# Optimization experiments

Hardware: AMD Instinct MI355X
Metric: run time of the kernel (lower is better)

## Reference

```python
import jax, jax.numpy as jnp
import numpy as np

N = 100_000      # nodes
D = 64           # in_dim
E = 1_600_000    # edges (avg degree 16)
P_L = 0.5        # leaky slope for low-pass gate
P_H = 0.5        # leaky slope for high-pass gate


def setup_inputs() -> dict:
    key = jax.random.key(0)
    ks = jax.random.split(key, 10)
    h = jax.random.normal(ks[0], (N, D), jnp.float32)
    d = jax.random.uniform(ks[1], (N,), jnp.float32)  # degree norms 1/sqrt(deg)
    src = jax.random.randint(ks[2], (E,), 0, N)
    dst = jax.random.randint(ks[3], (E,), 0, N)
    # xavier_normal(gain=1.414) scale ~ gain*sqrt(2/(fan_in+fan_out))
    sg = 1.414 * np.sqrt(2.0 / (2 * D + 1))
    sr = 1.414 * np.sqrt(2.0 / (2 * D + D))
    Wl = jax.random.normal(ks[4], (1, 2 * D), jnp.float32) * sg
    bl = jnp.zeros((1,), jnp.float32)
    Wh = jax.random.normal(ks[5], (1, 2 * D), jnp.float32) * sg
    bh = jnp.zeros((1,), jnp.float32)
    Wr = jax.random.normal(ks[6], (D, 2 * D), jnp.float32) * sr
    br = jnp.zeros((D,), jnp.float32)
    return {"h": h, "d": d, "src": src, "dst": dst,
            "Wl": Wl, "bl": bl, "Wh": Wh, "bh": bh, "Wr": Wr, "br": br}


def reference(h, d, src, dst, Wl, bl, Wh, bh, Wr, br):
    # gate_x(cat([h_dst, h_src])) == h_dst @ W[:, :D] + h_src @ W[:, D:] + b
    # -> project once per node [N], gather per edge [E] (avoids [E,2D] concat)
    low_dst = h @ Wl[0, :D]
    low_src = h @ Wl[0, D:]
    _low = low_dst[dst] + low_src[src] + bl[0]                     # [E]
    g_low = jnp.tanh(jax.nn.relu(jnp.where(_low > 0, _low, -P_L * _low)))

    high_dst = h @ Wh[0, :D]
    high_src = h @ Wh[0, D:]
    _high = high_dst[dst] + high_src[src] + bh[0]                  # [E]
    g_high = jnp.tanh(-jax.nn.relu(jnp.where(_high > 0, _high, -P_H * _high)))

    dd = d[dst] * d[src]                                           # [E]
    e_low = g_low * dd
    e_high = g_high * dd

    h_src = h[src]                                                 # [E, D]
    z_low = jax.ops.segment_sum(h_src * e_low[:, None], dst, num_segments=N)
    z_high = jax.ops.segment_sum(h_src * e_high[:, None], dst, num_segments=N)

    z = jnp.concatenate([z_low, z_high], axis=1)                   # [N, 2D]
    return z @ Wr.T + br                                           # [N, D]
```

## Files before the change

### kernel.cpp

```cpp
#include <hip/hip_runtime.h>
#include <hip/hip_fp16.h>
#include <math.h>

#define N_NODES 100000
#define D_DIM   64
#define N_EDGES 1600000
#define P_L 0.5f
#define P_H 0.5f

#define NPB   32
#define NB    3125
#define TILE  2048
#define NT    784
#define GRP   28
#define GT    28
#define CAPB  768
#define CAPH  512
#define ZS    132


typedef unsigned int uint;
typedef unsigned short ushort_t;
typedef float f2 __attribute__((ext_vector_type(2)));

__device__ inline ushort_t f2bf(float f) {
    uint u = __float_as_uint(f);
    uint r = (u + 0x7fffu + ((u >> 16) & 1u)) >> 16;
    return (ushort_t)r;
}

__device__ inline float tanh_pos(float x) {
    return 1.f - 2.f / (__expf(2.f * x) + 1.f);
}

__device__ inline void fma16(uint gy, uint4 hv, f2* acc) {
    float el = __half2float(__ushort_as_half((unsigned short)(gy & 0xffffu)));
    float eh = __half2float(__ushort_as_half((unsigned short)(gy >> 16)));
    f2 f01 = {__uint_as_float(hv.x << 16), __uint_as_float(hv.x & 0xffff0000u)};
    f2 f23 = {__uint_as_float(hv.y << 16), __uint_as_float(hv.y & 0xffff0000u)};
    f2 f45 = {__uint_as_float(hv.z << 16), __uint_as_float(hv.z & 0xffff0000u)};
    f2 f67 = {__uint_as_float(hv.w << 16), __uint_as_float(hv.w & 0xffff0000u)};
    acc[0] += f01 * el; acc[1] += f23 * el; acc[2] += f45 * el; acc[3] += f67 * el;
    acc[4] += f01 * eh; acc[5] += f23 * eh; acc[6] += f45 * eh; acc[7] += f67 * eh;
}

__device__ inline unsigned long long match4(int dl, bool active) {
    unsigned long long m = __ballot(active);
    #pragma unroll
    for (int b = 0; b < 4; ++b) {
        unsigned long long bal = __ballot(active && ((dl >> b) & 1));
        m &= ((dl >> b) & 1) ? bal : ~bal;
    }
    return m;
}

__global__ __launch_bounds__(256) void node_gates_kernel(
    const float* __restrict__ h, const float* __restrict__ dvec,
    const float* __restrict__ Wl, const float* __restrict__ Wh,
    ushort_t* __restrict__ hbf,
    float4* __restrict__ gdst4, float4* __restrict__ gsrc4)
{
    int tid = threadIdx.x;
    int lane = tid & 63;
    int half = lane >> 5;
    int l32 = lane & 31;
    int node = blockIdx.x * 8 + (tid >> 6) * 2 + half;

    float2 hv2 = *(const float2*)(h + (size_t)node * 64 + l32 * 2);
    uint pk = (uint)f2bf(hv2.x) | ((uint)f2bf(hv2.y) << 16);
    ((uint*)hbf)[(size_t)node * 32 + l32] = pk;

    float pld = hv2.x * Wl[2 * l32]      + hv2.y * Wl[2 * l32 + 1];
    float pls = hv2.x * Wl[64 + 2 * l32] + hv2.y * Wl[64 + 2 * l32 + 1];
    float phd = hv2.x * Wh[2 * l32]      + hv2.y * Wh[2 * l32 + 1];
    float phs = hv2.x * Wh[64 + 2 * l32] + hv2.y * Wh[64 + 2 * l32 + 1];
    #pragma unroll
    for (int m = 16; m >= 1; m >>= 1) {
        pld += __shfl_xor(pld, m);
        pls += __shfl_xor(pls, m);
        phd += __shfl_xor(phd, m);
        phs += __shfl_xor(phs, m);
    }
    if (l32 == 0) {
        float d = dvec[node];
        gdst4[node] = make_float4(pld, phd, d, 0.f);
        gsrc4[node] = make_float4(pls, phs, d, 0.f);
    }
}

__global__ __launch_bounds__(512) void bucket_hist_kernel(const int* __restrict__ dst,
                                                          int* __restrict__ T) {
    __shared__ int hist[NB];
    int tid = threadIdx.x;
    for (int i = tid; i < NB; i += 512) hist[i] = 0;
    __syncthreads();
    int base = blockIdx.x * TILE;
    #pragma unroll
    for (int j = 0; j < TILE / 512; ++j) {
        int e = base + j * 512 + tid;
        if (e < N_EDGES) atomicAdd(&hist[dst[e] >> 5], 1);
    }
    __syncthreads();
    int* row = T + (size_t)blockIdx.x * NB;
    for (int i = tid; i < NB; i += 512) row[i] = hist[i];
}

__global__ __launch_bounds__(1024) void scanA1_kernel(int* __restrict__ T,
                                                      int* __restrict__ S) {
    int b = blockIdx.x * 1024 + threadIdx.x;
    if (b >= NB) return;
    int g = blockIdx.y;
    int run = 0;
    #pragma unroll
    for (int w = g * GT; w < g * GT + GT; ++w) {
        int idx = w * NB + b;
        int v = T[idx];
        T[idx] = run;
        run += v;
    }
    S[(size_t)g * NB + b] = run;
}

__global__ __launch_bounds__(1024) void scanA2_kernel(int* __restrict__ S,
                                                      int* __restrict__ totG) {
    int b = blockIdx.x * 1024 + threadIdx.x;
    if (b >= NB) return;
    int run = 0;
    #pragma unroll
    for (int g = 0; g < GRP; ++g) {
        int idx = g * NB + b;
        int v = S[idx];
        S[idx] = run;
        run += v;
    }
    totG[b] = run;
}

__global__ __launch_bounds__(1024) void scanB_kernel(const int* __restrict__ totG,
                                                     int* __restrict__ baseG,
                                                     int* __restrict__ bucketoffs,
                                                     const float* __restrict__ Wr,
                                                     float* __restrict__ wrt) {
    int tid = threadIdx.x;
    for (int idx = tid; idx < 64 * 128; idx += 1024) {
        int c = idx >> 7;
        int k = idx & 127;
        wrt[k * 64 + c] = Wr[idx];
    }

    __shared__ int scan_lds[1024];
    int a[4];
    int s = 0;
    #pragma unroll
    for (int i = 0; i < 4; ++i) {
        int b = tid * 4 + i;
        a[i] = (b < NB) ? totG[b] : 0;
        s += a[i];
    }
    scan_lds[tid] = s;
    __syncthreads();
    for (int d = 1; d < 1024; d <<= 1) {
        int v = (tid >= d) ? scan_lds[tid - d] : 0;
        __syncthreads();
        scan_lds[tid] += v;
        __syncthreads();
    }
    int excl = scan_lds[tid] - s;
    int total = scan_lds[1023];
    #pragma unroll
    for (int i = 0; i < 4; ++i) {
        int b = tid * 4 + i;
        if (b < NB) { baseG[b] = excl; bucketoffs[b] = excl; }
        excl += a[i];
    }
    if (tid == 0) bucketoffs[NB] = total;
}

__global__ __launch_bounds__(512) void place_kernel(
    const int* __restrict__ src, const int* __restrict__ dst,
    const int* __restrict__ T, const int* __restrict__ S,
    const int* __restrict__ baseG,
    const float4* __restrict__ gdst4, const float4* __restrict__ gsrc4,
    const float* __restrict__ bl, const float* __restrict__ bh,
    uint2* __restrict__ ebuf)
{
    __shared__ int cur[NB];
    int tid = threadIdx.x;
    const int* row  = T + (size_t)blockIdx.x * NB;
    const int* Srow = S + (size_t)(blockIdx.x / GT) * NB;
    for (int i = tid; i < NB; i += 512) cur[i] = row[i] + Srow[i] + baseG[i];
    __syncthreads();

    float bl0 = bl[0], bh0 = bh[0];
    int base = blockIdx.x * TILE;
    #pragma unroll
    for (int j = 0; j < TILE / 512; ++j) {
        int e = base + j * 512 + tid;
        if (e >= N_EDGES) continue;
        int t = dst[e];
        int s = src[e];
        float4 gt = gdst4[t];
        float4 gs = gsrc4[s];
        float xl = gt.x + gs.x + bl0;
        float xh = gt.y + gs.y + bh0;
        float ll = xl > 0.f ? xl : -P_L * xl;
        float hh = xh > 0.f ? xh : -P_H * xh;
        float dd = gt.z * gs.z;
        float el =  tanh_pos(ll) * dd;
        float eh = -tanh_pos(hh) * dd;
        uint ge = (uint)__half_as_ushort(__float2half_rn(el))
                | ((uint)__half_as_ushort(__float2half_rn(eh)) << 16);
        int b  = t >> 5;
        uint dl = (uint)(t & 31);
        int pos = atomicAdd(&cur[b], 1);
        ebuf[pos] = make_uint2((uint)s | (dl << 17), ge);
    }
}

__global__ __launch_bounds__(256) void accum_final_kernel(
    const int* __restrict__ bucketoffs, const uint2* __restrict__ ebuf,
    const ushort_t* __restrict__ hbf, const float* __restrict__ wrt,
    const float* __restrict__ br, float* __restrict__ out)
{
    __shared__ float z[16 * ZS];
    __shared__ uint2 srec[CAPH];
    __shared__ int ncount[16];
    __shared__ int nbase[16];
    __shared__ int ncur[16];

    int tid = threadIdx.x;
    int lane = tid & 63;
    int bk = blockIdx.x >> 1;
    int hf = blockIdx.x & 1;
    int beg = bucketoffs[bk];
    int end = bucketoffs[bk + 1];
    int cnt = end - beg;
    if (cnt > CAPB) cnt = CAPB;

    if (tid < 16) ncount[tid] = 0;

    bool hA = tid < cnt;
    bool hB = tid + 256 < cnt;
    bool hC = tid + 512 < cnt;
    uint2 rA = hA ? ebuf[beg + tid]       : make_uint2(0, 0);
    uint2 rB = hB ? ebuf[beg + tid + 256] : make_uint2(0, 0);
    uint2 rC = hC ? ebuf[beg + tid + 512] : make_uint2(0, 0);
    __syncthreads();

    int dA5 = (int)((rA.x >> 17) & 31u);
    int dB5 = (int)((rB.x >> 17) & 31u);
    int dC5 = (int)((rC.x >> 17) & 31u);
    bool oA = hA && ((dA5 >> 4) == hf);
    bool oB = hB && ((dB5 >> 4) == hf);
    bool oC = hC && ((dC5 >> 4) == hf);
    int dlA = dA5 & 15, dlB = dB5 & 15, dlC = dC5 & 15;

    unsigned long long mA = match4(dlA, oA);
    if (oA && lane == (int)__builtin_ctzll(mA))
        atomicAdd(&ncount[dlA], (int)__popcll(mA));
    unsigned long long mB = match4(dlB, oB);
    if (oB && lane == (int)__builtin_ctzll(mB))
        atomicAdd(&ncount[dlB], (int)__popcll(mB));
    unsigned long long mC = match4(dlC, oC);
    if (oC && lane == (int)__builtin_ctzll(mC))
        atomicAdd(&ncount[dlC], (int)__popcll(mC));
    __syncthreads();

    if (tid < 16) {
        int v = ncount[tid];
        int p = v;
        #pragma unroll
        for (int d = 1; d < 16; d <<= 1) {
            int x = __shfl_up(p, d);
            if (tid >= d) p += x;
        }
        nbase[tid] = p - v;
        ncur[tid]  = p - v;
    }
    __syncthreads();

    if (oA) {
        int ldr = (int)__builtin_ctzll(mA);
        int base = 0;
        if (lane == ldr) base = atomicAdd(&ncur[dlA], (int)__popcll(mA));
        base = __shfl(base, ldr);
        int pos = base + (int)__popcll(mA & ((1ull << lane) - 1ull));
        if (pos < CAPH) srec[pos] = rA;
    }
    if (oB) {
        int ldr = (int)__builtin_ctzll(mB);
        int base = 0;
        if (lane == ldr) base = atomicAdd(&ncur[dlB], (int)__popcll(mB));
        base = __shfl(base, ldr);
        int pos = base + (int)__popcll(mB & ((1ull << lane) - 1ull));
        if (pos < CAPH) srec[pos] = rB;
    }
    if (oC) {
        int ldr = (int)__builtin_ctzll(mC);
        int base = 0;
        if (lane == ldr) base = atomicAdd(&ncur[dlC], (int)__popcll(mC));
        base = __shfl(base, ldr);
        int pos = base + (int)__popcll(mC & ((1ull << lane) - 1ull));
        if (pos < CAPH) srec[pos] = rC;
    }
    __syncthreads();

    int sg = tid >> 3;
    int l8 = tid & 7;
    int node4 = sg >> 1;
    int par = sg & 1;
    int rbeg = nbase[node4];
    int rend = ncur[node4];
    if (rend > CAPH) rend = CAPH;

    f2 acc[8];
    #pragma unroll
    for (int j = 0; j < 8; ++j) acc[j] = (f2){0.f, 0.f};

    int k = rbeg + par;
    for (; k + 6 < rend; k += 8) {
        uint2 r0 = srec[k];
        uint2 r1 = srec[k + 2];
        uint2 r2 = srec[k + 4];
        uint2 r3 = srec[k + 6];
        uint4 h0 = *(const uint4*)(hbf + (size_t)(r0.x & 0x1FFFF) * 64 + l8 * 8);
        uint4 h1 = *(const uint4*)(hbf + (size_t)(r1.x & 0x1FFFF) * 64 + l8 * 8);
        uint4 h2 = *(const uint4*)(hbf + (size_t)(r2.x & 0x1FFFF) * 64 + l8 * 8);
        uint4 h3 = *(const uint4*)(hbf + (size_t)(r3.x & 0x1FFFF) * 64 + l8 * 8);
        fma16(r0.y, h0, acc);
        fma16(r1.y, h1, acc);
        fma16(r2.y, h2, acc);
        fma16(r3.y, h3, acc);
    }
    for (; k < rend; k += 2) {
        uint2 r0 = srec[k];
        uint4 hv = *(const uint4*)(hbf + (size_t)(r0.x & 0x1FFFF) * 64 + l8 * 8);
        fma16(r0.y, hv, acc);
    }

    float* zp = &z[node4 * ZS + l8 * 8];
    if (par == 0) {
        *(float4*)(zp + 0)  = make_float4(acc[0].x, acc[0].y, acc[1].x, acc[1].y);
        *(float4*)(zp + 4)  = make_float4(acc[2].x, acc[2].y, acc[3].x, acc[3].y);
        *(float4*)(zp + 64) = make_float4(acc[4].x, acc[4].y, acc[5].x, acc[5].y);
        *(float4*)(zp + 68) = make_float4(acc[6].x, acc[6].y, acc[7].x, acc[7].y);
    }
    __syncthreads();
    if (par == 1) {
        float4 z0 = *(float4*)(zp + 0);
        float4 z1 = *(float4*)(zp + 4);
        float4 z2 = *(float4*)(zp + 64);
        float4 z3 = *(float4*)(zp + 68);
        *(float4*)(zp + 0)  = make_float4(z0.x + acc[0].x, z0.y + acc[0].y, z0.z + acc[1].x, z0.w + acc[1].y);
        *(float4*)(zp + 4)  = make_float4(z1.x + acc[2].x, z1.y + acc[2].y, z1.z + acc[3].x, z1.w + acc[3].y);
        *(float4*)(zp + 64) = make_float4(z2.x + acc[4].x, z2.y + acc[4].y, z2.z + acc[5].x, z2.w + acc[5].y);
        *(float4*)(zp + 68) = make_float4(z3.x + acc[6].x, z3.y + acc[6].y, z3.z + acc[7].x, z3.w + acc[7].y);
    }
    __syncthreads();

    int node = tid >> 4;
    int g = tid & 15;
    f2 fa0 = {0.f, 0.f}, fa1 = {0.f, 0.f};
    const float* zrow = z + node * ZS;
    #pragma unroll 2
    for (int kk = 0; kk < 128; kk += 4) {
        float4 z4 = *(const float4*)(zrow + kk);
        const float* wp = wrt + kk * 64 + g * 4;
        float4 w0 = *(const float4*)(wp);
        float4 w1 = *(const float4*)(wp + 64);
        float4 w2 = *(const float4*)(wp + 128);
        float4 w3 = *(const float4*)(wp + 192);
        fa0 += (f2){w0.x, w0.y} * z4.x; fa1 += (f2){w0.z, w0.w} * z4.x;
        fa0 += (f2){w1.x, w1.y} * z4.y; fa1 += (f2){w1.z, w1.w} * z4.y;
        fa0 += (f2){w2.x, w2.y} * z4.z; fa1 += (f2){w2.z, w2.w} * z4.z;
        fa0 += (f2){w3.x, w3.y} * z4.w; fa1 += (f2){w3.z, w3.w} * z4.w;
    }
    int n = bk * NPB + hf * 16 + node;
    float* op = out + (size_t)n * 64 + g * 4;
    const float* bp = br + g * 4;
    *(float4*)(op) = make_float4(fa0.x + bp[0], fa0.y + bp[1], fa1.x + bp[2], fa1.y + bp[3]);
}

extern "C" void kernel_launch(void* const* d_in, const int* in_sizes, int n_in,
                              void* d_out, int out_size, void* d_ws, size_t ws_size,
                              hipStream_t stream) {
    const float* h    = (const float*)d_in[0];
    const float* dvec = (const float*)d_in[1];
    const int*   src  = (const int*)  d_in[2];
    const int*   dst  = (const int*)  d_in[3];
    const float* Wl   = (const float*)d_in[4];
    const float* bl   = (const float*)d_in[5];
    const float* Wh   = (const float*)d_in[6];
    const float* bh   = (const float*)d_in[7];
    const float* Wr   = (const float*)d_in[8];
    const float* br   = (const float*)d_in[9];
    float* out = (float*)d_out;

    char* ws = (char*)d_ws;
    size_t off = 0;
    auto alloc = [&](size_t bytes) { char* p = ws + off; off += (bytes + 255) & ~size_t(255); return p; };

    ushort_t* hbf       = (ushort_t*)alloc((size_t)N_NODES * 64 * 2);
    float4*   gdst4     = (float4*)  alloc((size_t)N_NODES * 16);
    float4*   gsrc4     = (float4*)  alloc((size_t)N_NODES * 16);
    float*    wrt       = (float*)   alloc(64 * 128 * 4);
    int*      T         = (int*)     alloc((size_t)NT * NB * 4);
    int*      S         = (int*)     alloc((size_t)GRP * NB * 4);
    int*      totG      = (int*)     alloc((size_t)NB * 4);
    int*      baseG     = (int*)     alloc((size_t)NB * 4);
    int*      bucketoffs= (int*)     alloc((size_t)(NB + 1) * 4);
    uint2*    ebuf      = (uint2*)   alloc((size_t)N_EDGES * 8);

    node_gates_kernel<<<N_NODES / 8, 256, 0, stream>>>(h, dvec, Wl, Wh, hbf, gdst4, gsrc4);
    bucket_hist_kernel<<<NT, 512, 0, stream>>>(dst, T);
    {
        dim3 g1((NB + 1023) / 1024, GRP);
        scanA1_kernel<<<g1, 1024, 0, stream>>>(T, S);
    }
    scanA2_kernel<<<(NB + 1023) / 1024, 1024, 0, stream>>>(S, totG);
    scanB_kernel<<<1, 1024, 0, stream>>>(totG, baseG, bucketoffs, Wr, wrt);
    place_kernel<<<NT, 512, 0, stream>>>(src, dst, T, S, baseG, gdst4, gsrc4, bl, bh, ebuf);
    accum_final_kernel<<<NB * 2, 256, 0, stream>>>(bucketoffs, ebuf, hbf, wrt, br, out);
}
```

Measured before the change: 285.4 us.

## Replace tiled histogram and multi-pass scan with padded global atomic counters

The per-tile shared-memory histogram plus the two-level column scan is replaced by one global atomic count per bucket, padded to separate cache lines, and the counters are zeroed inside the node gates kernel. The placement pass then uses global atomics on those counters instead of precomputed per-tile offsets, which removes two kernels and the large T/S workspace traffic. In exchange, every edge now issues global atomics twice, and edge order within a bucket becomes nondeterministic. The accumulation loop also gains a 16-edge unrolled stage that issues eight gathers before their FMAs, adding memory-level parallelism at the cost of more registers.

After: 377.9 us. 32.4% more time.

```diff
diff --git a/kernel.cpp b/kernel.cpp
--- a/kernel.cpp
+++ b/kernel.cpp
@@ -10,13 +10,10 @@
 
 #define NPB   32
 #define NB    3125
-#define TILE  2048
-#define NT    784
-#define GRP   28
-#define GT    28
 #define CAPB  768
 #define CAPH  512
 #define ZS    132
+#define CPAD  16
 
 
 typedef unsigned int uint;
@@ -58,9 +55,15 @@
     const float* __restrict__ h, const float* __restrict__ dvec,
     const float* __restrict__ Wl, const float* __restrict__ Wh,
     ushort_t* __restrict__ hbf,
-    float4* __restrict__ gdst4, float4* __restrict__ gsrc4)
+    float4* __restrict__ gdst4, float4* __restrict__ gsrc4,
+    int* __restrict__ cursp)
 {
     int tid = threadIdx.x;
+    if (blockIdx.x < 13) {
+        int b = blockIdx.x * 256 + tid;
+        if (b < NB) cursp[b * CPAD] = 0;
+    }
+
     int lane = tid & 63;
     int half = lane >> 5;
     int l32 = lane & 31;
@@ -88,56 +91,13 @@
     }
 }
 
-__global__ __launch_bounds__(512) void bucket_hist_kernel(const int* __restrict__ dst,
-                                                          int* __restrict__ T) {
-    __shared__ int hist[NB];
-    int tid = threadIdx.x;
-    for (int i = tid; i < NB; i += 512) hist[i] = 0;
-    __syncthreads();
-    int base = blockIdx.x * TILE;
-    #pragma unroll
-    for (int j = 0; j < TILE / 512; ++j) {
-        int e = base + j * 512 + tid;
-        if (e < N_EDGES) atomicAdd(&hist[dst[e] >> 5], 1);
-    }
-    __syncthreads();
-    int* row = T + (size_t)blockIdx.x * NB;
-    for (int i = tid; i < NB; i += 512) row[i] = hist[i];
-}
-
-__global__ __launch_bounds__(1024) void scanA1_kernel(int* __restrict__ T,
-                                                      int* __restrict__ S) {
-    int b = blockIdx.x * 1024 + threadIdx.x;
-    if (b >= NB) return;
-    int g = blockIdx.y;
-    int run = 0;
-    #pragma unroll
-    for (int w = g * GT; w < g * GT + GT; ++w) {
-        int idx = w * NB + b;
-        int v = T[idx];
-        T[idx] = run;
-        run += v;
-    }
-    S[(size_t)g * NB + b] = run;
-}
-
-__global__ __launch_bounds__(1024) void scanA2_kernel(int* __restrict__ S,
-                                                      int* __restrict__ totG) {
-    int b = blockIdx.x * 1024 + threadIdx.x;
-    if (b >= NB) return;
-    int run = 0;
-    #pragma unroll
-    for (int g = 0; g < GRP; ++g) {
-        int idx = g * NB + b;
-        int v = S[idx];
-        S[idx] = run;
-        run += v;
-    }
-    totG[b] = run;
-}
-
-__global__ __launch_bounds__(1024) void scanB_kernel(const int* __restrict__ totG,
-                                                     int* __restrict__ baseG,
+__global__ __launch_bounds__(512) void count_kernel(const int* __restrict__ dst,
+                                                    int* __restrict__ cursp) {
+    int e = blockIdx.x * 512 + threadIdx.x;
+    atomicAdd(&cursp[(dst[e] >> 5) * CPAD], 1);
+}
+
+__global__ __launch_bounds__(1024) void scanB_kernel(int* __restrict__ cursp,
                                                      int* __restrict__ bucketoffs,
                                                      const float* __restrict__ Wr,
                                                      float* __restrict__ wrt) {
@@ -154,7 +114,7 @@
     #pragma unroll
     for (int i = 0; i < 4; ++i) {
         int b = tid * 4 + i;
-        a[i] = (b < NB) ? totG[b] : 0;
+        a[i] = (b < NB) ? cursp[b * CPAD] : 0;
         s += a[i];
     }
     scan_lds[tid] = s;
@@ -170,7 +130,7 @@
     #pragma unroll
     for (int i = 0; i < 4; ++i) {
         int b = tid * 4 + i;
-        if (b < NB) { baseG[b] = excl; bucketoffs[b] = excl; }
+        if (b < NB) { bucketoffs[b] = excl; cursp[b * CPAD] = excl; }
         excl += a[i];
     }
     if (tid == 0) bucketoffs[NB] = total;
@@ -178,43 +138,28 @@
 
 __global__ __launch_bounds__(512) void place_kernel(
     const int* __restrict__ src, const int* __restrict__ dst,
-    const int* __restrict__ T, const int* __restrict__ S,
-    const int* __restrict__ baseG,
     const float4* __restrict__ gdst4, const float4* __restrict__ gsrc4,
     const float* __restrict__ bl, const float* __restrict__ bh,
-    uint2* __restrict__ ebuf)
+    int* __restrict__ cursp, uint2* __restrict__ ebuf)
 {
-    __shared__ int cur[NB];
-    int tid = threadIdx.x;
-    const int* row  = T + (size_t)blockIdx.x * NB;
-    const int* Srow = S + (size_t)(blockIdx.x / GT) * NB;
-    for (int i = tid; i < NB; i += 512) cur[i] = row[i] + Srow[i] + baseG[i];
-    __syncthreads();
-
-    float bl0 = bl[0], bh0 = bh[0];
-    int base = blockIdx.x * TILE;
-    #pragma unroll
-    for (int j = 0; j < TILE / 512; ++j) {
-        int e = base + j * 512 + tid;
-        if (e >= N_EDGES) continue;
-        int t = dst[e];
-        int s = src[e];
-        float4 gt = gdst4[t];
-        float4 gs = gsrc4[s];
-        float xl = gt.x + gs.x + bl0;
-        float xh = gt.y + gs.y + bh0;
-        float ll = xl > 0.f ? xl : -P_L * xl;
-        float hh = xh > 0.f ? xh : -P_H * xh;
-        float dd = gt.z * gs.z;
-        float el =  tanh_pos(ll) * dd;
-        float eh = -tanh_pos(hh) * dd;
-        uint ge = (uint)__half_as_ushort(__float2half_rn(el))
-                | ((uint)__half_as_ushort(__float2half_rn(eh)) << 16);
-        int b  = t >> 5;
-        uint dl = (uint)(t & 31);
-        int pos = atomicAdd(&cur[b], 1);
-        ebuf[pos] = make_uint2((uint)s | (dl << 17), ge);
-    }
+    int e = blockIdx.x * 512 + threadIdx.x;
+    int t = dst[e];
+    int s = src[e];
+    float4 gt = gdst4[t];
+    float4 gs = gsrc4[s];
+    float xl = gt.x + gs.x + bl[0];
+    float xh = gt.y + gs.y + bh[0];
+    float ll = xl > 0.f ? xl : -P_L * xl;
+    float hh = xh > 0.f ? xh : -P_H * xh;
+    float dd = gt.z * gs.z;
+    float el =  tanh_pos(ll) * dd;
+    float eh = -tanh_pos(hh) * dd;
+    uint ge = (uint)__half_as_ushort(__float2half_rn(el))
+            | ((uint)__half_as_ushort(__float2half_rn(eh)) << 16);
+    int b  = t >> 5;
+    uint dl = (uint)(t & 31);
+    int pos = atomicAdd(&cursp[b * CPAD], 1);
+    ebuf[pos] = make_uint2((uint)s | (dl << 17), ge);
 }
 
 __global__ __launch_bounds__(256) void accum_final_kernel(
@@ -318,6 +263,17 @@
     for (int j = 0; j < 8; ++j) acc[j] = (f2){0.f, 0.f};
 
     int k = rbeg + par;
+    for (; k + 14 < rend; k += 16) {
+        uint gy[8]; uint4 hh[8];
+        #pragma unroll
+        for (int i = 0; i < 8; ++i) {
+            uint2 r = srec[k + 2 * i];
+            gy[i] = r.y;
+            hh[i] = *(const uint4*)(hbf + (size_t)(r.x & 0x1FFFF) * 64 + l8 * 8);
+        }
+        #pragma unroll
+        for (int i = 0; i < 8; ++i) fma16(gy[i], hh[i], acc);
+    }
     for (; k + 6 < rend; k += 8) {
         uint2 r0 = srec[k];
         uint2 r1 = srec[k + 2];
@@ -404,21 +360,13 @@
     float4*   gdst4     = (float4*)  alloc((size_t)N_NODES * 16);
     float4*   gsrc4     = (float4*)  alloc((size_t)N_NODES * 16);
     float*    wrt       = (float*)   alloc(64 * 128 * 4);
-    int*      T         = (int*)     alloc((size_t)NT * NB * 4);
-    int*      S         = (int*)     alloc((size_t)GRP * NB * 4);
-    int*      totG      = (int*)     alloc((size_t)NB * 4);
-    int*      baseG     = (int*)     alloc((size_t)NB * 4);
+    int*      cursp     = (int*)     alloc((size_t)NB * CPAD * 4);
     int*      bucketoffs= (int*)     alloc((size_t)(NB + 1) * 4);
     uint2*    ebuf      = (uint2*)   alloc((size_t)N_EDGES * 8);
 
-    node_gates_kernel<<<N_NODES / 8, 256, 0, stream>>>(h, dvec, Wl, Wh, hbf, gdst4, gsrc4);
-    bucket_hist_kernel<<<NT, 512, 0, stream>>>(dst, T);
-    {
-        dim3 g1((NB + 1023) / 1024, GRP);
-        scanA1_kernel<<<g1, 1024, 0, stream>>>(T, S);
-    }
-    scanA2_kernel<<<(NB + 1023) / 1024, 1024, 0, stream>>>(S, totG);
-    scanB_kernel<<<1, 1024, 0, stream>>>(totG, baseG, bucketoffs, Wr, wrt);
-    place_kernel<<<NT, 512, 0, stream>>>(src, dst, T, S, baseG, gdst4, gsrc4, bl, bh, ebuf);
+    node_gates_kernel<<<N_NODES / 8, 256, 0, stream>>>(h, dvec, Wl, Wh, hbf, gdst4, gsrc4, cursp);
+    count_kernel<<<N_EDGES / 512, 512, 0, stream>>>(dst, cursp);
+    scanB_kernel<<<1, 1024, 0, stream>>>(cursp, bucketoffs, Wr, wrt);
+    place_kernel<<<N_EDGES / 512, 512, 0, stream>>>(src, dst, gdst4, gsrc4, bl, bh, cursp, ebuf);
     accum_final_kernel<<<NB * 2, 256, 0, stream>>>(bucketoffs, ebuf, hbf, wrt, br, out);
 }
```

## Pre-project node features through Wr before edge aggregation

Applied to the files above, without the earlier changes.

Uses linearity to move the output projection ahead of the scatter. Each node's features are multiplied by the two 64x64 halves of Wr up front and stored as fp16 (128 values per node). The per-edge gather then accumulates these projected rows directly, so the per-block LDS z buffer, its two barriers and the final small matmul go away. In exchange the gathered row per edge doubles from 128 to 256 bytes, a separate weight-reshuffle kernel is added, and storage switches from bf16 to fp16, which changes precision and overflow behaviour.

Measured after the change: 330.5 us. 15.8% more time.

```diff
diff --git a/kernel.cpp b/kernel.cpp
--- a/kernel.cpp
+++ b/kernel.cpp
@@ -16,32 +16,29 @@
 #define GT    28
 #define CAPB  768
 #define CAPH  512
-#define ZS    132
 
 
 typedef unsigned int uint;
 typedef unsigned short ushort_t;
 typedef float f2 __attribute__((ext_vector_type(2)));
 
-__device__ inline ushort_t f2bf(float f) {
-    uint u = __float_as_uint(f);
-    uint r = (u + 0x7fffu + ((u >> 16) & 1u)) >> 16;
-    return (ushort_t)r;
-}
-
 __device__ inline float tanh_pos(float x) {
     return 1.f - 2.f / (__expf(2.f * x) + 1.f);
 }
 
-__device__ inline void fma16(uint gy, uint4 hv, f2* acc) {
+__device__ inline f2 cvt2(uint u) {
+    __half2 h = *reinterpret_cast<const __half2*>(&u);
+    float2 f = __half22float2(h);
+    return (f2){f.x, f.y};
+}
+
+__device__ inline void fmaAB(uint gy, uint4 ha, uint4 hb, f2* acc) {
     float el = __half2float(__ushort_as_half((unsigned short)(gy & 0xffffu)));
     float eh = __half2float(__ushort_as_half((unsigned short)(gy >> 16)));
-    f2 f01 = {__uint_as_float(hv.x << 16), __uint_as_float(hv.x & 0xffff0000u)};
-    f2 f23 = {__uint_as_float(hv.y << 16), __uint_as_float(hv.y & 0xffff0000u)};
-    f2 f45 = {__uint_as_float(hv.z << 16), __uint_as_float(hv.z & 0xffff0000u)};
-    f2 f67 = {__uint_as_float(hv.w << 16), __uint_as_float(hv.w & 0xffff0000u)};
-    acc[0] += f01 * el; acc[1] += f23 * el; acc[2] += f45 * el; acc[3] += f67 * el;
-    acc[4] += f01 * eh; acc[5] += f23 * eh; acc[6] += f45 * eh; acc[7] += f67 * eh;
+    acc[0] += cvt2(ha.x) * el + cvt2(hb.x) * eh;
+    acc[1] += cvt2(ha.y) * el + cvt2(hb.y) * eh;
+    acc[2] += cvt2(ha.z) * el + cvt2(hb.z) * eh;
+    acc[3] += cvt2(ha.w) * el + cvt2(hb.w) * eh;
 }
 
 __device__ inline unsigned long long match4(int dl, bool active) {
@@ -57,18 +54,21 @@
 __global__ __launch_bounds__(256) void node_gates_kernel(
     const float* __restrict__ h, const float* __restrict__ dvec,
     const float* __restrict__ Wl, const float* __restrict__ Wh,
-    ushort_t* __restrict__ hbf,
+    const float* __restrict__ W2,
+    ushort_t* __restrict__ hab,
     float4* __restrict__ gdst4, float4* __restrict__ gsrc4)
 {
+    __shared__ float hlds[8][64];
     int tid = threadIdx.x;
     int lane = tid & 63;
     int half = lane >> 5;
     int l32 = lane & 31;
-    int node = blockIdx.x * 8 + (tid >> 6) * 2 + half;
+    int nl = (tid >> 6) * 2 + half;
+    int node = blockIdx.x * 8 + nl;
 
     float2 hv2 = *(const float2*)(h + (size_t)node * 64 + l32 * 2);
-    uint pk = (uint)f2bf(hv2.x) | ((uint)f2bf(hv2.y) << 16);
-    ((uint*)hbf)[(size_t)node * 32 + l32] = pk;
+    hlds[nl][2 * l32]     = hv2.x;
+    hlds[nl][2 * l32 + 1] = hv2.y;
 
     float pld = hv2.x * Wl[2 * l32]      + hv2.y * Wl[2 * l32 + 1];
     float pls = hv2.x * Wl[64 + 2 * l32] + hv2.y * Wl[64 + 2 * l32 + 1];
@@ -85,6 +85,34 @@
         float d = dvec[node];
         gdst4[node] = make_float4(pld, phd, d, 0.f);
         gsrc4[node] = make_float4(pls, phs, d, 0.f);
+    }
+    __syncthreads();
+
+    int c0 = l32 * 4;
+    f2 a01 = {0.f, 0.f}, a23 = {0.f, 0.f};
+    const float* hrow = hlds[nl];
+    #pragma unroll 4
+    for (int k = 0; k < 64; k += 2) {
+        float2 hk = *(const float2*)(hrow + k);
+        float4 w0 = *(const float4*)(W2 + (size_t)k * 128 + c0);
+        float4 w1 = *(const float4*)(W2 + (size_t)(k + 1) * 128 + c0);
+        a01 += (f2){w0.x, w0.y} * hk.x; a23 += (f2){w0.z, w0.w} * hk.x;
+        a01 += (f2){w1.x, w1.y} * hk.y; a23 += (f2){w1.z, w1.w} * hk.y;
+    }
+    __half2 p0 = __float22half2_rn(make_float2(a01.x, a01.y));
+    __half2 p1 = __float22half2_rn(make_float2(a23.x, a23.y));
+    uint2 pk;
+    pk.x = *reinterpret_cast<uint*>(&p0);
+    pk.y = *reinterpret_cast<uint*>(&p1);
+    *(uint2*)(hab + (size_t)node * 128 + c0) = pk;
+}
+
+__global__ __launch_bounds__(1024) void w2_kernel(const float* __restrict__ Wr,
+                                                  float* __restrict__ W2) {
+    for (int idx = threadIdx.x; idx < 64 * 128; idx += 1024) {
+        int k = idx >> 7;
+        int c = idx & 127;
+        W2[idx] = (c < 64) ? Wr[c * 128 + k] : Wr[(c - 64) * 128 + 64 + k];
     }
 }
 
@@ -138,16 +166,8 @@
 
 __global__ __launch_bounds__(1024) void scanB_kernel(const int* __restrict__ totG,
                                                      int* __restrict__ baseG,
-                                                     int* __restrict__ bucketoffs,
-                                                     const float* __restrict__ Wr,
-                                                     float* __restrict__ wrt) {
+                                                     int* __restrict__ bucketoffs) {
     int tid = threadIdx.x;
-    for (int idx = tid; idx < 64 * 128; idx += 1024) {
-        int c = idx >> 7;
-        int k = idx & 127;
-        wrt[k * 64 + c] = Wr[idx];
-    }
-
     __shared__ int scan_lds[1024];
     int a[4];
     int s = 0;
@@ -219,10 +239,9 @@
 
 __global__ __launch_bounds__(256) void accum_final_kernel(
     const int* __restrict__ bucketoffs, const uint2* __restrict__ ebuf,
-    const ushort_t* __restrict__ hbf, const float* __restrict__ wrt,
-    const float* __restrict__ br, float* __restrict__ out)
+    const ushort_t* __restrict__ hab, const float* __restrict__ br,
+    float* __restrict__ out)
 {
-    __shared__ float z[16 * ZS];
     __shared__ uint2 srec[CAPH];
     __shared__ int ncount[16];
     __shared__ int nbase[16];
@@ -313,9 +332,9 @@
     int rend = ncur[node4];
     if (rend > CAPH) rend = CAPH;
 
-    f2 acc[8];
-    #pragma unroll
-    for (int j = 0; j < 8; ++j) acc[j] = (f2){0.f, 0.f};
+    f2 acc[4];
+    #pragma unroll
+    for (int j = 0; j < 4; ++j) acc[j] = (f2){0.f, 0.f};
 
     int k = rbeg + par;
     for (; k + 6 < rend; k += 8) {
@@ -323,62 +342,52 @@
         uint2 r1 = srec[k + 2];
         uint2 r2 = srec[k + 4];
         uint2 r3 = srec[k + 6];
-        uint4 h0 = *(const uint4*)(hbf + (size_t)(r0.x & 0x1FFFF) * 64 + l8 * 8);
-        uint4 h1 = *(const uint4*)(hbf + (size_t)(r1.x & 0x1FFFF) * 64 + l8 * 8);
-        uint4 h2 = *(const uint4*)(hbf + (size_t)(r2.x & 0x1FFFF) * 64 + l8 * 8);
-        uint4 h3 = *(const uint4*)(hbf + (size_t)(r3.x & 0x1FFFF) * 64 + l8 * 8);
-        fma16(r0.y, h0, acc);
-        fma16(r1.y, h1, acc);
-        fma16(r2.y, h2, acc);
-        fma16(r3.y, h3, acc);
+        const ushort_t* p0 = hab + (size_t)(r0.x & 0x1FFFF) * 128 + l8 * 8;
+        const ushort_t* p1 = hab + (size_t)(r1.x & 0x1FFFF) * 128 + l8 * 8;
+        const ushort_t* p2 = hab + (size_t)(r2.x & 0x1FFFF) * 128 + l8 * 8;
+        const ushort_t* p3 = hab + (size_t)(r3.x & 0x1FFFF) * 128 + l8 * 8;
+        uint4 a0 = *(const uint4*)(p0);
+        uint4 b0 = *(const uint4*)(p0 + 64);
+        uint4 a1 = *(const uint4*)(p1);
+        uint4 b1 = *(const uint4*)(p1 + 64);
+        uint4 a2 = *(const uint4*)(p2);
+        uint4 b2 = *(const uint4*)(p2 + 64);
+        uint4 a3 = *(const uint4*)(p3);
+        uint4 b3 = *(const uint4*)(p3 + 64);
+        fmaAB(r0.y, a0, b0, acc);
+        fmaAB(r1.y, a1, b1, acc);
+        fmaAB(r2.y, a2, b2, acc);
+        fmaAB(r3.y, a3, b3, acc);
     }
     for (; k < rend; k += 2) {
         uint2 r0 = srec[k];
-        uint4 hv = *(const uint4*)(hbf + (size_t)(r0.x & 0x1FFFF) * 64 + l8 * 8);
-        fma16(r0.y, hv, acc);
-    }
-
-    float* zp = &z[node4 * ZS + l8 * 8];
+        const ushort_t* p0 = hab + (size_t)(r0.x & 0x1FFFF) * 128 + l8 * 8;
+        uint4 a0 = *(const uint4*)(p0);
+        uint4 b0 = *(const uint4*)(p0 + 64);
+        fmaAB(r0.y, a0, b0, acc);
+    }
+
+    f2 oth[4];
+    #pragma unroll
+    for (int j = 0; j < 4; ++j) {
+        oth[j].x = __shfl_xor(acc[j].x, 8);
+        oth[j].y = __shfl_xor(acc[j].y, 8);
+    }
     if (par == 0) {
-        *(float4*)(zp + 0)  = make_float4(acc[0].x, acc[0].y, acc[1].x, acc[1].y);
-        *(float4*)(zp + 4)  = make_float4(acc[2].x, acc[2].y, acc[3].x, acc[3].y);
-        *(float4*)(zp + 64) = make_float4(acc[4].x, acc[4].y, acc[5].x, acc[5].y);
-        *(float4*)(zp + 68) = make_float4(acc[6].x, acc[6].y, acc[7].x, acc[7].y);
-    }
-    __syncthreads();
-    if (par == 1) {
-        float4 z0 = *(float4*)(zp + 0);
-        float4 z1 = *(float4*)(zp + 4);
-        float4 z2 = *(float4*)(zp + 64);
-        float4 z3 = *(float4*)(zp + 68);
-        *(float4*)(zp + 0)  = make_float4(z0.x + acc[0].x, z0.y + acc[0].y, z0.z + acc[1].x, z0.w + acc[1].y);
-        *(float4*)(zp + 4)  = make_float4(z1.x + acc[2].x, z1.y + acc[2].y, z1.z + acc[3].x, z1.w + acc[3].y);
-        *(float4*)(zp + 64) = make_float4(z2.x + acc[4].x, z2.y + acc[4].y, z2.z + acc[5].x, z2.w + acc[5].y);
-        *(float4*)(zp + 68) = make_float4(z3.x + acc[6].x, z3.y + acc[6].y, z3.z + acc[7].x, z3.w + acc[7].y);
-    }
-    __syncthreads();
-
-    int node = tid >> 4;
-    int g = tid & 15;
-    f2 fa0 = {0.f, 0.f}, fa1 = {0.f, 0.f};
-    const float* zrow = z + node * ZS;
-    #pragma unroll 2
-    for (int kk = 0; kk < 128; kk += 4) {
-        float4 z4 = *(const float4*)(zrow + kk);
-        const float* wp = wrt + kk * 64 + g * 4;
-        float4 w0 = *(const float4*)(wp);
-        float4 w1 = *(const float4*)(wp + 64);
-        float4 w2 = *(const float4*)(wp + 128);
-        float4 w3 = *(const float4*)(wp + 192);
-        fa0 += (f2){w0.x, w0.y} * z4.x; fa1 += (f2){w0.z, w0.w} * z4.x;
-        fa0 += (f2){w1.x, w1.y} * z4.y; fa1 += (f2){w1.z, w1.w} * z4.y;
-        fa0 += (f2){w2.x, w2.y} * z4.z; fa1 += (f2){w2.z, w2.w} * z4.z;
-        fa0 += (f2){w3.x, w3.y} * z4.w; fa1 += (f2){w3.z, w3.w} * z4.w;
-    }
-    int n = bk * NPB + hf * 16 + node;
-    float* op = out + (size_t)n * 64 + g * 4;
-    const float* bp = br + g * 4;
-    *(float4*)(op) = make_float4(fa0.x + bp[0], fa0.y + bp[1], fa1.x + bp[2], fa1.y + bp[3]);
+        int n = bk * NPB + hf * 16 + node4;
+        const float* bp = br + l8 * 8;
+        float4 b0 = *(const float4*)(bp);
+        float4 b1 = *(const float4*)(bp + 4);
+        float* op = out + (size_t)n * 64 + l8 * 8;
+        *(float4*)(op) = make_float4(acc[0].x + oth[0].x + b0.x,
+                                     acc[0].y + oth[0].y + b0.y,
+                                     acc[1].x + oth[1].x + b0.z,
+                                     acc[1].y + oth[1].y + b0.w);
+        *(float4*)(op + 4) = make_float4(acc[2].x + oth[2].x + b1.x,
+                                         acc[2].y + oth[2].y + b1.y,
+                                         acc[3].x + oth[3].x + b1.z,
+                                         acc[3].y + oth[3].y + b1.w);
+    }
 }
 
 extern "C" void kernel_launch(void* const* d_in, const int* in_sizes, int n_in,
@@ -400,10 +409,10 @@
     size_t off = 0;
     auto alloc = [&](size_t bytes) { char* p = ws + off; off += (bytes + 255) & ~size_t(255); return p; };
 
-    ushort_t* hbf       = (ushort_t*)alloc((size_t)N_NODES * 64 * 2);
+    ushort_t* hab       = (ushort_t*)alloc((size_t)N_NODES * 128 * 2);
     float4*   gdst4     = (float4*)  alloc((size_t)N_NODES * 16);
     float4*   gsrc4     = (float4*)  alloc((size_t)N_NODES * 16);
-    float*    wrt       = (float*)   alloc(64 * 128 * 4);
+    float*    W2        = (float*)   alloc(64 * 128 * 4);
     int*      T         = (int*)     alloc((size_t)NT * NB * 4);
     int*      S         = (int*)     alloc((size_t)GRP * NB * 4);
     int*      totG      = (int*)     alloc((size_t)NB * 4);
@@ -411,14 +420,15 @@
     int*      bucketoffs= (int*)     alloc((size_t)(NB + 1) * 4);
     uint2*    ebuf      = (uint2*)   alloc((size_t)N_EDGES * 8);
 
-    node_gates_kernel<<<N_NODES / 8, 256, 0, stream>>>(h, dvec, Wl, Wh, hbf, gdst4, gsrc4);
+    w2_kernel<<<1, 1024, 0, stream>>>(Wr, W2);
+    node_gates_kernel<<<N_NODES / 8, 256, 0, stream>>>(h, dvec, Wl, Wh, W2, hab, gdst4, gsrc4);
     bucket_hist_kernel<<<NT, 512, 0, stream>>>(dst, T);
     {
         dim3 g1((NB + 1023) / 1024, GRP);
         scanA1_kernel<<<g1, 1024, 0, stream>>>(T, S);
     }
     scanA2_kernel<<<(NB + 1023) / 1024, 1024, 0, stream>>>(S, totG);
-    scanB_kernel<<<1, 1024, 0, stream>>>(totG, baseG, bucketoffs, Wr, wrt);
+    scanB_kernel<<<1, 1024, 0, stream>>>(totG, baseG, bucketoffs);
     place_kernel<<<NT, 512, 0, stream>>>(src, dst, T, S, baseG, gdst4, gsrc4, bl, bh, ebuf);
-    accum_final_kernel<<<NB * 2, 256, 0, stream>>>(bucketoffs, ebuf, hbf, wrt, br, out);
-}
+    accum_final_kernel<<<NB * 2, 256, 0, stream>>>(bucketoffs, ebuf, hab, br, out);
+}
```
